# Performance work log

Hardware: AMD Instinct MI355X
Metric: run time of the kernel (lower is better)

## Reference

```python
import jax, jax.numpy as jnp
import numpy as np
from jax import lax

K = 3; KK = K * K; S = 1; P = 1; D = 1
BN_EPS = 1e-5


def setup_inputs() -> dict:
    key = jax.random.key(0)
    ks = jax.random.split(key, 4)
    B, C, H, W = 8, 128, 64, 64
    cout = 128
    # xavier-ish scales for conv weights
    def xavier(k, shape):
        fan_in = shape[1] * shape[2] * shape[3]
        fan_out = shape[0] * shape[2] * shape[3]
        limit = np.sqrt(6.0 / (fan_in + fan_out))
        return jax.random.uniform(k, shape, jnp.float32, -limit, limit)
    return {
        "x": jax.random.normal(ks[0], (B, C, H, W), jnp.float32),
        "w_off": xavier(ks[1], (2 * KK, C, K, K)),
        "b_off": jnp.zeros((2 * KK,), jnp.float32),
        "w_mod": xavier(ks[2], (KK, C, K, K)),
        "b_mod": jnp.zeros((KK,), jnp.float32),
        "w_reg": xavier(ks[3], (cout, C, K, K)),
        "b_reg": jnp.zeros((cout,), jnp.float32),
        "gamma": jnp.ones((cout,), jnp.float32),
        "beta": jnp.zeros((cout,), jnp.float32),
    }


def _conv(x, w, b):
    y = lax.conv_general_dilated(x, w, (S, S), [(P, P), (P, P)],
                                 rhs_dilation=(D, D),
                                 dimension_numbers=("NCHW", "OIHW", "NCHW"))
    return y + b[None, :, None, None]


def _deform_conv(x, offset, mask, w_reg, b_reg):
    B, C, H, W = x.shape
    Ho, Wo = offset.shape[2], offset.shape[3]
    # torchvision layout: [B, 2*KK, Ho, Wo], interleaved (dy, dx) per tap
    off = offset.reshape(B, KK, 2, Ho, Wo)
    dy, dx = off[:, :, 0], off[:, :, 1]                      # [B,KK,Ho,Wo]
    ki = jnp.arange(KK) // K
    kj = jnp.arange(KK) % K
    base_y = (jnp.arange(Ho) * S - P)[None, :, None] + (ki * D)[:, None, None]  # [KK,Ho,1]
    base_x = (jnp.arange(Wo) * S - P)[None, None, :] + (kj * D)[:, None, None]  # [KK,1,Wo]
    py = base_y[None].astype(x.dtype) + dy                   # [B,KK,Ho,Wo]
    px = base_x[None].astype(x.dtype) + dx

    y0f = jnp.floor(py); x0f = jnp.floor(px)
    ly = py - y0f; lx = px - x0f
    y0 = y0f.astype(jnp.int32); x0 = x0f.astype(jnp.int32)
    y1 = y0 + 1; x1 = x0 + 1

    def gather(iy, ix):
        valid = ((iy >= 0) & (iy < H) & (ix >= 0) & (ix < W)).astype(x.dtype)
        iyc = jnp.clip(iy, 0, H - 1)
        ixc = jnp.clip(ix, 0, W - 1)
        v = jax.vmap(lambda img, a, b: img[:, a, b])(x, iyc, ixc)  # [B,C,KK,Ho,Wo]
        return v * valid[:, None]

    val = (gather(y0, x0) * ((1 - ly) * (1 - lx))[:, None]
           + gather(y0, x1) * ((1 - ly) * lx)[:, None]
           + gather(y1, x0) * (ly * (1 - lx))[:, None]
           + gather(y1, x1) * (ly * lx)[:, None])               # [B,C,KK,Ho,Wo]

    patches = val * mask[:, None]                               # modulated samples
    wr = w_reg.reshape(w_reg.shape[0], C, KK)
    out = jnp.einsum("ock,bckhw->bohw", wr, patches)
    return out + b_reg[None, :, None, None]


def reference(x, w_off, b_off, w_mod, b_mod, w_reg, b_reg, gamma, beta):
    offset = _conv(x, w_off, b_off)
    modulator = 2.0 * jax.nn.sigmoid(_conv(x, w_mod, b_mod))
    y = _deform_conv(x, offset, modulator, w_reg, b_reg)
    # BatchNorm2d (training-mode batch statistics) + ReLU
    mu = y.mean(axis=(0, 2, 3), keepdims=True)
    var = y.var(axis=(0, 2, 3), keepdims=True)
    y = (y - mu) * lax.rsqrt(var + BN_EPS)
    y = y * gamma[None, :, None, None] + beta[None, :, None, None]
    return jax.nn.relu(y)
```

## Files before the change

### kernel.cpp

```cpp
#include <hip/hip_runtime.h>
#include <math.h>

#define H 64
#define W 64
#define C 128
#define NB 8
#define COUT 128
#define HWi 4096
#define NKC 36
#define PADu 40

typedef __attribute__((ext_vector_type(8))) short short8;
typedef __attribute__((ext_vector_type(8))) unsigned short ushort8;
typedef __attribute__((ext_vector_type(4))) unsigned int uint4v;
typedef __attribute__((ext_vector_type(4))) float f32x4;

__device__ __forceinline__ unsigned short f2bf(float f){
    unsigned u = __float_as_uint(f);
    unsigned r = (u + 0x7FFFu + ((u >> 16) & 1u)) >> 16;
    return (unsigned short)r;
}
__device__ __forceinline__ float bf2f(unsigned short u){
    return __uint_as_float(((unsigned)u) << 16);
}
__device__ __forceinline__ unsigned cvtpk_bf16(float lo, float hi){
    unsigned r;
    asm("v_cvt_pk_bf16_f32 %0, %1, %2" : "=v"(r) : "v"(lo), "v"(hi));
    return r;
}

__global__ void k_pre(const float* __restrict__ x, unsigned short* __restrict__ xTp,
                      const float* __restrict__ w_reg, const float* __restrict__ w_off,
                      const float* __restrict__ w_mod, const float* __restrict__ b_off,
                      const float* __restrict__ b_mod,
                      unsigned short* __restrict__ wAv, unsigned short* __restrict__ w27A,
                      float* __restrict__ biasom, float* __restrict__ psum){
    int tid = threadIdx.x;
    if (blockIdx.x >= 528){
        int i = (blockIdx.x - 528) * 256 + tid;
        if (i < 147456){
            int kc = i >> 12, rem = i & 4095;
            int q = rem >> 10, r = (rem >> 3) & 127, j = rem & 7;
            int kk = kc * 32 + q * 8 + j, k = kk >> 7, c = kk & 127;
            wAv[i] = f2bf(w_reg[r * 1152 + c * 9 + k]);
        } else if (i < 147456 + 36864){
            int j2 = i - 147456;
            int kc = j2 >> 10, rem = j2 & 1023;
            int q = rem >> 8, m = (rem >> 3) & 31, t = rem & 7;
            int kkl = q * 8 + t;
            int kk = kc * 32 + kkl, k = kk >> 7, c = kk & 127;
            float v = 0.f;
            if (m < 18) v = w_off[m * 1152 + c * 9 + k];
            else if (m < 27) v = w_mod[(m - 18) * 1152 + c * 9 + k];
            w27A[j2] = f2bf(v);
        } else if (i < 147456 + 36864 + 32){
            int m = i - 147456 - 36864;
            biasom[m] = (m < 18) ? b_off[m] : (m < 27 ? b_mod[m - 18] : 0.f);
        } else if (i < 147456 + 36864 + 32 + 256){
            psum[i - 147456 - 36864 - 32] = 0.f;
        }
        return;
    }
    int bidx = blockIdx.x;
    int b = bidx & 7, hp = bidx >> 3;
    unsigned short* row = xTp + (size_t)(b * 66 + hp) * 66 * 128;
    if (hp == 0 || hp == 65){
        ushort8 z = {0,0,0,0,0,0,0,0};
        for (int i = tid; i < 66 * 128 / 8; i += 256) ((ushort8*)row)[i] = z;
        return;
    }
    int h = hp - 1;
    __shared__ unsigned short s[64 * 136];
    int w = tid & 63, c0 = tid >> 6;
    for (int cc = 0; cc < 128; cc += 4){
        int c = cc + c0;
        s[w * 136 + c] = f2bf(x[(size_t)(b * 128 + c) * HWi + h * 64 + w]);
    }
    __syncthreads();
    if (tid < 32){
        ushort8 z = {0,0,0,0,0,0,0,0};
        int wp = (tid < 16) ? 0 : 65;
        int sg = tid & 15;
        *(ushort8*)(row + wp * 128 + sg * 8) = z;
    }
    for (int it = tid; it < 1024; it += 256){
        int w2 = it >> 4, sg = it & 15;
        *(ushort8*)(row + (w2 + 1) * 128 + sg * 8) = *(const ushort8*)(s + w2 * 136 + sg * 8);
    }
}

__global__ __launch_bounds__(512, 4) void k_fused(const unsigned short* __restrict__ xTp,
        const unsigned short* __restrict__ w27A, const float* __restrict__ biasom,
        const unsigned short* __restrict__ wAv, const float* __restrict__ b_reg,
        unsigned short* __restrict__ ybf, float* __restrict__ psum){
    __shared__ char smem[38912];
    int tid = threadIdx.x;
    int lb = (blockIdx.x & 7) * 64 + (blockIdx.x >> 3);
    int n0 = lb * 64;
    int b = n0 >> 12, h = (n0 >> 6) & 63;

    {
        int grp = tid >> 8, gt = tid & 255;
        unsigned short* pB = (unsigned short*)(smem + grp * 10240);
        int wvg = gt >> 6, lane = gt & 63, quad = lane >> 4, l16 = lane & 15;
        int nl = gt >> 2, sg = gt & 3;
        f32x4 acc0 = {0.f,0.f,0.f,0.f}, acc1 = {0.f,0.f,0.f,0.f};
        int kc0 = grp * 18;
        auto p1load = [&](int i, ushort8& B8){
            int kc = kc0 + i;
            int k = kc >> 2, cb = (kc & 3) << 5;
            int ki = k / 3, kj = k - ki * 3;
            int rowi = (b * 66 + h + ki) * 66 + (nl + kj);
            B8 = *(const ushort8*)(xTp + (size_t)rowi * 128 + cb + sg * 8);
        };
        auto p1body = [&](int i, ushort8& B8){
            int p = i & 1;
            int kc = kc0 + i;
            const unsigned short* wj = w27A + kc * 1024 + quad * 256;
            short8 a0 = *(const short8*)(wj + l16 * 8);
            short8 a1 = *(const short8*)(wj + (16 + l16) * 8);
            *(ushort8*)(pB + p * 2560 + nl * PADu + sg * 8) = B8;
            if (i + 2 < 18) p1load(i + 2, B8);
            __syncthreads();
            short8 bfrag = *(const short8*)(pB + p * 2560 + (wvg * 16 + l16) * PADu + quad * 8);
            acc0 = __builtin_amdgcn_mfma_f32_16x16x32_bf16(a0, bfrag, acc0, 0, 0, 0);
            acc1 = __builtin_amdgcn_mfma_f32_16x16x32_bf16(a1, bfrag, acc1, 0, 0, 0);
        };
        ushort8 rB0, rB1;
        p1load(0, rB0);
        p1load(1, rB1);
        for (int ih = 0; ih < 9; ih++){
            p1body(ih * 2,     rB0);
            p1body(ih * 2 + 1, rB1);
        }
        float* s_red = (float*)(smem + 20480);
        int npx = wvg * 16 + l16;
        if (grp == 1){
            #pragma unroll
            for (int t = 0; t < 2; t++){
                f32x4 a = t ? acc1 : acc0;
                #pragma unroll
                for (int r = 0; r < 4; r++)
                    s_red[npx * 32 + t * 16 + quad * 4 + r] = a[r];
            }
        }
        __syncthreads();
        if (grp == 0){
            unsigned short* s_OM = (unsigned short*)smem;
            #pragma unroll
            for (int t = 0; t < 2; t++){
                f32x4 a = t ? acc1 : acc0;
                #pragma unroll
                for (int r = 0; r < 4; r++){
                    int oc = t * 16 + quad * 4 + r;
                    float v = a[r] + s_red[npx * 32 + oc] + biasom[oc];
                    if (oc >= 18) v = 2.f / (1.f + expf(-v));
                    s_OM[npx * 32 + oc] = f2bf(v);
                }
            }
        }
        __syncthreads();
    }

    unsigned short* sB = (unsigned short*)smem;
    int*   s_a0 = (int*)(smem + 20480);
    float* s_w0 = (float*)(smem + 29696);
    const unsigned short* s_OM = (const unsigned short*)smem;

    for (int idx = tid; idx < 576; idx += 512){
        int k = idx >> 6, px_ = idx & 63;
        float dy = bf2f(s_OM[px_ * 32 + 2 * k]);
        float dx = bf2f(s_OM[px_ * 32 + 2 * k + 1]);
        float m  = bf2f(s_OM[px_ * 32 + 18 + k]);
        int ki = k / 3, kj = k - ki * 3;
        float py  = (float)(h - 1 + ki) + dy;
        float pxf = (float)(px_ - 1 + kj) + dx;
        float y0f = floorf(py), x0f = floorf(pxf);
        float ly = py - y0f, lx = pxf - x0f;
        int iy0 = (int)y0f, ix0 = (int)x0f;
        int cy0 = min(max(iy0 + 1, 0), 65), cy1 = min(max(iy0 + 2, 0), 65);
        int cx0 = min(max(ix0 + 1, 0), 65), cx1 = min(max(ix0 + 2, 0), 65);
        int rb = b * 66 * 66;
        s_a0[0 * 576 + idx] = ((rb + cy0 * 66) + cx0) * 128;
        s_a0[1 * 576 + idx] = ((rb + cy0 * 66) + cx1) * 128;
        s_a0[2 * 576 + idx] = ((rb + cy1 * 66) + cx0) * 128;
        s_a0[3 * 576 + idx] = ((rb + cy1 * 66) + cx1) * 128;
        s_w0[0 * 576 + idx] = (1.f - ly) * (1.f - lx) * m;
        s_w0[1 * 576 + idx] = (1.f - ly) * lx * m;
        s_w0[2 * 576 + idx] = ly * (1.f - lx) * m;
        s_w0[3 * 576 + idx] = ly * lx * m;
    }
    __syncthreads();

    int wv = tid >> 6, lane = tid & 63, quad = lane >> 4, l16 = lane & 15;
    int ocq = wv & 3, ng = wv >> 2;
    int px = tid >> 3, cg = tid & 7;

    int rowA0 = ocq * 32 + l16, rowA1 = rowA0 + 16;
    int offB0 = (ng * 32 + l16) * PADu + quad * 8;
    int offB1 = (ng * 32 + 16 + l16) * PADu + quad * 8;

    f32x4 acc00 = {0.f,0.f,0.f,0.f}, acc01 = {0.f,0.f,0.f,0.f};
    f32x4 acc10 = {0.f,0.f,0.f,0.f}, acc11 = {0.f,0.f,0.f,0.f};

    auto loadP = [&](int j, ushort8& C0, ushort8& C1, ushort8& C2, ushort8& C3, float4& Wt){
        int k = j >> 1, cb = (j & 1) << 6;
        int idx = k * 64 + px;
        int co = cb + cg * 8;
        Wt.x = s_w0[0 * 576 + idx]; Wt.y = s_w0[1 * 576 + idx];
        Wt.z = s_w0[2 * 576 + idx]; Wt.w = s_w0[3 * 576 + idx];
        C0 = *(const ushort8*)(xTp + s_a0[0 * 576 + idx] + co);
        C1 = *(const ushort8*)(xTp + s_a0[1 * 576 + idx] + co);
        C2 = *(const ushort8*)(xTp + s_a0[2 * 576 + idx] + co);
        C3 = *(const ushort8*)(xTp + s_a0[3 * 576 + idx] + co);
    };
    auto bodyP = [&](int j, ushort8& C0, ushort8& C1, ushort8& C2, ushort8& C3, float4& Wt){
        int p = j & 1;
        unsigned short* sBp = sB + p * 5120;
        const unsigned short* wj = wAv + (size_t)(2 * j) * 4096 + quad * 1024;
        short8 a00 = *(const short8*)(wj + rowA0 * 8);
        short8 a01 = *(const short8*)(wj + rowA1 * 8);
        short8 a10 = *(const short8*)(wj + 4096 + rowA0 * 8);
        short8 a11 = *(const short8*)(wj + 4096 + rowA1 * 8);
        uint4v ov;
        #pragma unroll
        for (int q = 0; q < 4; q++){
            float v0 = Wt.x * bf2f(C0[2*q])   + Wt.y * bf2f(C1[2*q])
                     + Wt.z * bf2f(C2[2*q])   + Wt.w * bf2f(C3[2*q]);
            float v1 = Wt.x * bf2f(C0[2*q+1]) + Wt.y * bf2f(C1[2*q+1])
                     + Wt.z * bf2f(C2[2*q+1]) + Wt.w * bf2f(C3[2*q+1]);
            ov[q] = cvtpk_bf16(v0, v1);
        }
        *(uint4v*)(sBp + (cg >> 2) * 2560 + px * PADu + (cg & 3) * 8) = ov;
        if (j + 2 < 18) loadP(j + 2, C0, C1, C2, C3, Wt);
        __syncthreads();
        short8 b0 = *(const short8*)(sBp + offB0);
        short8 b1 = *(const short8*)(sBp + offB1);
        acc00 = __builtin_amdgcn_mfma_f32_16x16x32_bf16(a00, b0, acc00, 0, 0, 0);
        acc01 = __builtin_amdgcn_mfma_f32_16x16x32_bf16(a00, b1, acc01, 0, 0, 0);
        acc10 = __builtin_amdgcn_mfma_f32_16x16x32_bf16(a01, b0, acc10, 0, 0, 0);
        acc11 = __builtin_amdgcn_mfma_f32_16x16x32_bf16(a01, b1, acc11, 0, 0, 0);
        b0 = *(const short8*)(sBp + 2560 + offB0);
        b1 = *(const short8*)(sBp + 2560 + offB1);
        acc00 = __builtin_amdgcn_mfma_f32_16x16x32_bf16(a10, b0, acc00, 0, 0, 0);
        acc01 = __builtin_amdgcn_mfma_f32_16x16x32_bf16(a10, b1, acc01, 0, 0, 0);
        acc10 = __builtin_amdgcn_mfma_f32_16x16x32_bf16(a11, b0, acc10, 0, 0, 0);
        acc11 = __builtin_amdgcn_mfma_f32_16x16x32_bf16(a11, b1, acc11, 0, 0, 0);
    };

    ushort8 C0a, C1a, C2a, C3a, C0b, C1b, C2b, C3b;
    float4 Wta, Wtb;
    loadP(0, C0a, C1a, C2a, C3a, Wta);
    loadP(1, C0b, C1b, C2b, C3b, Wtb);
    for (int jh = 0; jh < 9; jh++){
        bodyP(jh * 2,     C0a, C1a, C2a, C3a, Wta);
        bodyP(jh * 2 + 1, C0b, C1b, C2b, C3b, Wtb);
    }

    __syncthreads();
    float* ls = (float*)smem;
    int sp0 = h * 64;
    #pragma unroll
    for (int to = 0; to < 2; to++){
        #pragma unroll
        for (int tn = 0; tn < 2; tn++){
            f32x4 a = to ? (tn ? acc11 : acc10) : (tn ? acc01 : acc00);
            int nl = ng * 32 + tn * 16 + l16;
            #pragma unroll
            for (int r = 0; r < 4; r++){
                int oc = ocq * 32 + to * 16 + quad * 4 + r;
                float v = a[r] + b_reg[oc];
                ybf[(size_t)(b * 128 + oc) * HWi + sp0 + nl] = f2bf(v);
                ls[oc * 67 + nl] = v;
            }
        }
    }
    __syncthreads();
    if (tid < 128){
        int oc = tid;
        float s = 0.f, s2 = 0.f;
        #pragma unroll 8
        for (int nl = 0; nl < 64; nl++){
            float v = ls[oc * 67 + nl];
            s += v; s2 = fmaf(v, v, s2);
        }
        atomicAdd(&psum[oc], s);
        atomicAdd(&psum[128 + oc], s2);
    }
}

__global__ void k_apply(const unsigned short* __restrict__ ybf, const float* __restrict__ psum,
                        const float* __restrict__ gamma, const float* __restrict__ beta,
                        float* __restrict__ out){
    int lb = ((int)blockIdx.x & 7) * 256 + ((int)blockIdx.x >> 3);
    int e8 = (lb * 256 + (int)threadIdx.x) * 8;
    int c = (e8 >> 12) & 127;
    ushort8 u = *(const ushort8*)(ybf + e8);
    float s = psum[c], s2 = psum[128 + c];
    float mean = s * (1.f / 32768.f);
    float var  = s2 * (1.f / 32768.f) - mean * mean;
    float rs = rsqrtf(var + 1e-5f);
    float g = gamma[c] * rs;
    float bt = beta[c] - mean * g;
    float4 lo, hi;
    lo.x = fmaxf(fmaf(bf2f(u[0]), g, bt), 0.f);
    lo.y = fmaxf(fmaf(bf2f(u[1]), g, bt), 0.f);
    lo.z = fmaxf(fmaf(bf2f(u[2]), g, bt), 0.f);
    lo.w = fmaxf(fmaf(bf2f(u[3]), g, bt), 0.f);
    hi.x = fmaxf(fmaf(bf2f(u[4]), g, bt), 0.f);
    hi.y = fmaxf(fmaf(bf2f(u[5]), g, bt), 0.f);
    hi.z = fmaxf(fmaf(bf2f(u[6]), g, bt), 0.f);
    hi.w = fmaxf(fmaf(bf2f(u[7]), g, bt), 0.f);
    *(float4*)(out + e8)     = lo;
    *(float4*)(out + e8 + 4) = hi;
}

extern "C" void kernel_launch(void* const* d_in, const int* in_sizes, int n_in,
                              void* d_out, int out_size, void* d_ws, size_t ws_size,
                              hipStream_t stream){
    const float* x     = (const float*)d_in[0];
    const float* w_off = (const float*)d_in[1];
    const float* b_off = (const float*)d_in[2];
    const float* w_mod = (const float*)d_in[3];
    const float* b_mod = (const float*)d_in[4];
    const float* w_reg = (const float*)d_in[5];
    const float* b_reg = (const float*)d_in[6];
    const float* gamma = (const float*)d_in[7];
    const float* beta  = (const float*)d_in[8];

    char* wsb = (char*)d_ws;
    unsigned short* xTp   = (unsigned short*)(wsb);
    unsigned short* ybf   = (unsigned short*)(wsb + 11018240);
    unsigned short* wAv   = (unsigned short*)(wsb + 19406848);
    unsigned short* w27A  = (unsigned short*)(wsb + 19701760);
    float*          biasom= (float*)(wsb + 19775488);
    float*          psum  = (float*)(wsb + 19775616);
    float* out = (float*)d_out;

    hipLaunchKernelGGL(k_pre,   dim3(1250), dim3(256), 0, stream, x, xTp, w_reg, w_off, w_mod, b_off, b_mod, wAv, w27A, biasom, psum);
    hipLaunchKernelGGL(k_fused, dim3(512),  dim3(512), 0, stream, xTp, w27A, biasom, wAv, b_reg, ybf, psum);
    hipLaunchKernelGGL(k_apply, dim3(2048), dim3(256), 0, stream, ybf, psum, gamma, beta, out);
}
```

Before: 130.3 us.

## Fuse BN apply into main kernel via grid-wide atomic barrier

Drops the separate BN/ReLU kernel and the bf16 intermediate tensor. Each fused block keeps its conv output tile in shared memory, waits on a global atomic counter until all 512 blocks have added their partial statistics, then normalises and writes fp32 output directly. This removes one launch and a round-trip of the intermediate through HBM. It relies on all 512 blocks being co-resident (launch bounds 512,4 on 256 CUs) to avoid deadlock, and adds spin-wait time at the barrier.

Result: slower. 208.1 us (+59.7%).

```diff
diff --git a/kernel.cpp b/kernel.cpp
--- a/kernel.cpp
+++ b/kernel.cpp
@@ -9,6 +9,7 @@
 #define HWi 4096
 #define NKC 36
 #define PADu 40
+#define NBLK 512u
 
 typedef __attribute__((ext_vector_type(8))) short short8;
 typedef __attribute__((ext_vector_type(8))) unsigned short ushort8;
@@ -34,7 +35,8 @@
                       const float* __restrict__ w_mod, const float* __restrict__ b_off,
                       const float* __restrict__ b_mod,
                       unsigned short* __restrict__ wAv, unsigned short* __restrict__ w27A,
-                      float* __restrict__ biasom, float* __restrict__ psum){
+                      float* __restrict__ biasom, float* __restrict__ psum,
+                      unsigned* __restrict__ bar){
     int tid = threadIdx.x;
     if (blockIdx.x >= 528){
         int i = (blockIdx.x - 528) * 256 + tid;
@@ -56,8 +58,10 @@
         } else if (i < 147456 + 36864 + 32){
             int m = i - 147456 - 36864;
             biasom[m] = (m < 18) ? b_off[m] : (m < 27 ? b_mod[m - 18] : 0.f);
-        } else if (i < 147456 + 36864 + 32 + 256){
-            psum[i - 147456 - 36864 - 32] = 0.f;
+        } else if (i < 147456 + 36864 + 32 + 257){
+            int z = i - (147456 + 36864 + 32);
+            if (z < 256) psum[z] = 0.f;
+            else *bar = 0u;
         }
         return;
     }
@@ -92,7 +96,8 @@
 __global__ __launch_bounds__(512, 4) void k_fused(const unsigned short* __restrict__ xTp,
         const unsigned short* __restrict__ w27A, const float* __restrict__ biasom,
         const unsigned short* __restrict__ wAv, const float* __restrict__ b_reg,
-        unsigned short* __restrict__ ybf, float* __restrict__ psum){
+        const float* __restrict__ gamma, const float* __restrict__ beta,
+        float* __restrict__ out, float* __restrict__ psum, unsigned* __restrict__ bar){
     __shared__ char smem[38912];
     int tid = threadIdx.x;
     int lb = (blockIdx.x & 7) * 64 + (blockIdx.x >> 3);
@@ -194,7 +199,7 @@
 
     int wv = tid >> 6, lane = tid & 63, quad = lane >> 4, l16 = lane & 15;
     int ocq = wv & 3, ng = wv >> 2;
-    int px = tid >> 3, cg = tid & 7;
+    int px = tid >> 3, cg2 = tid & 7;
 
     int rowA0 = ocq * 32 + l16, rowA1 = rowA0 + 16;
     int offB0 = (ng * 32 + l16) * PADu + quad * 8;
@@ -206,7 +211,7 @@
     auto loadP = [&](int j, ushort8& C0, ushort8& C1, ushort8& C2, ushort8& C3, float4& Wt){
         int k = j >> 1, cb = (j & 1) << 6;
         int idx = k * 64 + px;
-        int co = cb + cg * 8;
+        int co = cb + cg2 * 8;
         Wt.x = s_w0[0 * 576 + idx]; Wt.y = s_w0[1 * 576 + idx];
         Wt.z = s_w0[2 * 576 + idx]; Wt.w = s_w0[3 * 576 + idx];
         C0 = *(const ushort8*)(xTp + s_a0[0 * 576 + idx] + co);
@@ -231,7 +236,7 @@
                      + Wt.z * bf2f(C2[2*q+1]) + Wt.w * bf2f(C3[2*q+1]);
             ov[q] = cvtpk_bf16(v0, v1);
         }
-        *(uint4v*)(sBp + (cg >> 2) * 2560 + px * PADu + (cg & 3) * 8) = ov;
+        *(uint4v*)(sBp + (cg2 >> 2) * 2560 + px * PADu + (cg2 & 3) * 8) = ov;
         if (j + 2 < 18) loadP(j + 2, C0, C1, C2, C3, Wt);
         __syncthreads();
         short8 b0 = *(const short8*)(sBp + offB0);
@@ -259,7 +264,6 @@
 
     __syncthreads();
     float* ls = (float*)smem;
-    int sp0 = h * 64;
     #pragma unroll
     for (int to = 0; to < 2; to++){
         #pragma unroll
@@ -269,9 +273,7 @@
             #pragma unroll
             for (int r = 0; r < 4; r++){
                 int oc = ocq * 32 + to * 16 + quad * 4 + r;
-                float v = a[r] + b_reg[oc];
-                ybf[(size_t)(b * 128 + oc) * HWi + sp0 + nl] = f2bf(v);
-                ls[oc * 67 + nl] = v;
+                ls[oc * 67 + nl] = a[r] + b_reg[oc];
             }
         }
     }
@@ -287,32 +289,34 @@
         atomicAdd(&psum[oc], s);
         atomicAdd(&psum[128 + oc], s2);
     }
-}
-
-__global__ void k_apply(const unsigned short* __restrict__ ybf, const float* __restrict__ psum,
-                        const float* __restrict__ gamma, const float* __restrict__ beta,
-                        float* __restrict__ out){
-    int lb = ((int)blockIdx.x & 7) * 256 + ((int)blockIdx.x >> 3);
-    int e8 = (lb * 256 + (int)threadIdx.x) * 8;
-    int c = (e8 >> 12) & 127;
-    ushort8 u = *(const ushort8*)(ybf + e8);
-    float s = psum[c], s2 = psum[128 + c];
+
+    __syncthreads();
+    if (tid == 0){
+        __hip_atomic_fetch_add(bar, 1u, __ATOMIC_ACQ_REL, __HIP_MEMORY_SCOPE_AGENT);
+        while (__hip_atomic_load(bar, __ATOMIC_ACQUIRE, __HIP_MEMORY_SCOPE_AGENT) < NBLK)
+            __builtin_amdgcn_s_sleep(2);
+    }
+    __syncthreads();
+
+    int oc2 = tid >> 2, q4 = tid & 3;
+    float s  = __hip_atomic_load(&psum[oc2],       __ATOMIC_RELAXED, __HIP_MEMORY_SCOPE_AGENT);
+    float s2 = __hip_atomic_load(&psum[128 + oc2], __ATOMIC_RELAXED, __HIP_MEMORY_SCOPE_AGENT);
     float mean = s * (1.f / 32768.f);
     float var  = s2 * (1.f / 32768.f) - mean * mean;
     float rs = rsqrtf(var + 1e-5f);
-    float g = gamma[c] * rs;
-    float bt = beta[c] - mean * g;
-    float4 lo, hi;
-    lo.x = fmaxf(fmaf(bf2f(u[0]), g, bt), 0.f);
-    lo.y = fmaxf(fmaf(bf2f(u[1]), g, bt), 0.f);
-    lo.z = fmaxf(fmaf(bf2f(u[2]), g, bt), 0.f);
-    lo.w = fmaxf(fmaf(bf2f(u[3]), g, bt), 0.f);
-    hi.x = fmaxf(fmaf(bf2f(u[4]), g, bt), 0.f);
-    hi.y = fmaxf(fmaf(bf2f(u[5]), g, bt), 0.f);
-    hi.z = fmaxf(fmaf(bf2f(u[6]), g, bt), 0.f);
-    hi.w = fmaxf(fmaf(bf2f(u[7]), g, bt), 0.f);
-    *(float4*)(out + e8)     = lo;
-    *(float4*)(out + e8 + 4) = hi;
+    float g = gamma[oc2] * rs;
+    float bt = beta[oc2] - mean * g;
+    float* op = out + (size_t)(b * 128 + oc2) * HWi + h * 64 + q4 * 16;
+    const float* lr = ls + oc2 * 67 + q4 * 16;
+    #pragma unroll
+    for (int r = 0; r < 4; r++){
+        float4 o;
+        o.x = fmaxf(fmaf(lr[r * 4 + 0], g, bt), 0.f);
+        o.y = fmaxf(fmaf(lr[r * 4 + 1], g, bt), 0.f);
+        o.z = fmaxf(fmaf(lr[r * 4 + 2], g, bt), 0.f);
+        o.w = fmaxf(fmaf(lr[r * 4 + 3], g, bt), 0.f);
+        *(float4*)(op + r * 4) = o;
+    }
 }
 
 extern "C" void kernel_launch(void* const* d_in, const int* in_sizes, int n_in,
@@ -330,14 +334,13 @@
 
     char* wsb = (char*)d_ws;
     unsigned short* xTp   = (unsigned short*)(wsb);
-    unsigned short* ybf   = (unsigned short*)(wsb + 11018240);
     unsigned short* wAv   = (unsigned short*)(wsb + 19406848);
     unsigned short* w27A  = (unsigned short*)(wsb + 19701760);
     float*          biasom= (float*)(wsb + 19775488);
     float*          psum  = (float*)(wsb + 19775616);
+    unsigned*       bar   = (unsigned*)(wsb + 19776640);
     float* out = (float*)d_out;
 
-    hipLaunchKernelGGL(k_pre,   dim3(1250), dim3(256), 0, stream, x, xTp, w_reg, w_off, w_mod, b_off, b_mod, wAv, w27A, biasom, psum);
-    hipLaunchKernelGGL(k_fused, dim3(512),  dim3(512), 0, stream, xTp, w27A, biasom, wAv, b_reg, ybf, psum);
-    hipLaunchKernelGGL(k_apply, dim3(2048), dim3(256), 0, stream, ybf, psum, gamma, beta, out);
-}
+    hipLaunchKernelGGL(k_pre, dim3(1250), dim3(256), 0, stream, x, xTp, w_reg, w_off, w_mod, b_off, b_mod, wAv, w27A, biasom, psum, bar);
+    hipLaunchKernelGGL(k_fused, dim3(512), dim3(512), 0, stream, xTp, w27A, biasom, wAv, b_reg, gamma, beta, out, psum, bar);
+}
```
